# Performance work log

Measured on AMD Instinct MI355X. Metric: run time of the kernel, lower is better.

The kernel has to match this reference:

```python
import jax, jax.numpy as jnp
import numpy as np

NUM_HEADS = 16

def _alibi(S, H, dtype):
    # fairseq-style ALiBi: slopes[h] * -(|i-j|), H assumed power of 2
    start = 2.0 ** (-8.0 / H)
    slopes = start ** jnp.arange(1, H + 1, dtype=jnp.float32)      # [H]
    pos = jnp.arange(S)
    rel = -jnp.abs(pos[None, :] - pos[:, None]).astype(jnp.float32)  # [S,S]
    return (slopes[:, None, None] * rel).astype(dtype)             # [H,S,S]

def setup_inputs() -> dict:
    key = jax.random.key(0)
    kx, km, kw1, kw2 = jax.random.split(key, 4)
    B, S, D = 2, 2048, 1024
    inputs = jax.random.normal(kx, (B, S, D), dtype=jnp.float32)
    mask = jax.random.bernoulli(km, 0.9, (B, S))
    mask = mask.at[:, 0].set(True)  # ensure each row has a valid key
    Wqkv = jax.random.normal(kw1, (3 * D, D), dtype=jnp.float32) * 0.02
    bqkv = jnp.zeros((3 * D,), dtype=jnp.float32)
    Wproj = jax.random.normal(kw2, (D, D), dtype=jnp.float32) * 0.02
    bproj = jnp.zeros((D,), dtype=jnp.float32)
    return {"inputs": inputs, "mask": mask, "Wqkv": Wqkv, "bqkv": bqkv,
            "Wproj": Wproj, "bproj": bproj}

def reference(inputs, mask, Wqkv, bqkv, Wproj, bproj):
    B, S, D = inputs.shape
    H = NUM_HEADS
    dh = D // H
    scale = D ** (-0.5)  # NOTE: original scales by full dim, not head dim
    qkv = inputs @ Wqkv.T + bqkv                       # [B,S,3D]
    qkv = qkv.reshape(B, S, H, 3 * dh).transpose(0, 2, 1, 3)  # [B,H,S,3dh]
    q, k, v = qkv[..., :dh], qkv[..., dh:2 * dh], qkv[..., 2 * dh:]
    attn = jnp.einsum('bhqd,bhkd->bhqk', q, k) * scale  # [B,H,S,S]
    attn = attn + _alibi(S, H, attn.dtype)[None]
    attn = jnp.where(mask[:, None, None, :], attn, jnp.finfo(attn.dtype).min)
    attn = jax.nn.softmax(attn, axis=-1)
    x = jnp.einsum('bhqk,bhkd->bhqd', attn, v)          # [B,H,S,dh]
    x = x.transpose(0, 2, 1, 3).reshape(B, S, D)
    return x @ Wproj.T + bproj
```

## Files before the change

### kernel.cpp

```cpp
#include <hip/hip_runtime.h>
#include <cstdint>
#include <cstddef>

#define B_  2
#define S_  2048
#define D_  1024
#define H_  16
#define DH_ 64
#define M_  (B_*S_)
#define N3_ (3*D_)
#define NT_ (S_/64)

typedef float f32x4 __attribute__((ext_vector_type(4)));
typedef short short8 __attribute__((ext_vector_type(8)));
typedef unsigned short u16x8 __attribute__((ext_vector_type(8)));
typedef unsigned short u16x4 __attribute__((ext_vector_type(4)));
typedef unsigned short u16x2 __attribute__((ext_vector_type(2)));

__device__ __forceinline__ unsigned short f2bf(float x) {
    unsigned int u = __float_as_uint(x);
    unsigned int r = (u + 0x7FFFu + ((u >> 16) & 1u)) >> 16;
    return (unsigned short)r;
}

__device__ __forceinline__ float exp2_(float x) { return __builtin_amdgcn_exp2f(x); }

__device__ __forceinline__ unsigned int cvt_pk_bf16(float a, float b) {
    unsigned int r;
    asm volatile("v_cvt_pk_bf16_f32 %0, %1, %2" : "=v"(r) : "v"(a), "v"(b));
    return r;
}

__device__ __forceinline__ void gload16(const void* g, void* l) {
    __builtin_amdgcn_global_load_lds(
        (const __attribute__((address_space(1))) unsigned int*)g,
        (__attribute__((address_space(3))) unsigned int*)l,
        16, 0, 0);
}

__global__ void k_detect_mask(const unsigned char* __restrict__ mb, int* __restrict__ flag) {
    __shared__ int sBig, sM4, sM8;
    if (threadIdx.x == 0) { sBig = 0; sM4 = 0; sM8 = 0; }
    __syncthreads();
    int big = 0, m4 = 0, m8 = 0;
    for (int i = threadIdx.x; i < 4096; i += blockDim.x) {
        unsigned char v = mb[i];
        if (v > 1) big = 1;
        if (v && (i & 3)) m4 = 1;
        if (v && ((i & 7) == 4)) m8 = 1;
    }
    if (big) atomicOr(&sBig, 1);
    if (m4)  atomicOr(&sM4, 1);
    if (m8)  atomicOr(&sM8, 1);
    __syncthreads();
    if (threadIdx.x == 0) {
        int w;
        if (sBig)      w = 0;
        else if (sM4)  w = 1;
        else if (sM8)  w = 4;
        else           w = 8;
        *flag = w;
    }
}

__global__ void k_expand_mask(const void* __restrict__ mask, const int* __restrict__ flag,
                              float* __restrict__ maskbias, int n) {
    int i = blockIdx.x * blockDim.x + threadIdx.x;
    if (i >= n) return;
    int w = *flag;
    bool on;
    if (w == 0)      on = ((const float*)mask)[i] != 0.0f;
    else if (w == 1) on = ((const unsigned char*)mask)[i] != 0;
    else if (w == 4) on = ((const int*)mask)[i] != 0;
    else             on = ((const long long*)mask)[i] != 0;
    maskbias[i] = on ? 0.0f : -1e30f;
}

__global__ void k_f2bf(const float* __restrict__ in, unsigned short* __restrict__ out, int n) {
    int i = (blockIdx.x * blockDim.x + threadIdx.x) * 4;
    if (i >= n) return;
    float4 v = *reinterpret_cast<const float4*>(&in[i]);
    u16x4 o = { f2bf(v.x), f2bf(v.y), f2bf(v.z), f2bf(v.w) };
    *reinterpret_cast<u16x4*>(&out[i]) = o;
}

template <bool OUT_BF16>
__global__ __launch_bounds__(256) void k_gemm_bf16_nt(
    const unsigned short* __restrict__ A, const unsigned short* __restrict__ W,
    const float* __restrict__ bias, void* __restrict__ Cout,
    int M, int N, int K) {
    __shared__ __align__(16) unsigned short Al[128 * 64];
    __shared__ __align__(16) unsigned short Wl[128 * 64];

    const int tid  = threadIdx.x;
    const int lane = tid & 63;
    const int w    = tid >> 6;
    const int wr   = w >> 1, wc = w & 1;
    const int l16  = lane & 15, g = lane >> 4;
    const int m0 = blockIdx.y * 128, n0 = blockIdx.x * 128;

    f32x4 acc[4][4];
#pragma unroll
    for (int m = 0; m < 4; ++m)
#pragma unroll
        for (int n = 0; n < 4; ++n) acc[m][n] = (f32x4){0.f, 0.f, 0.f, 0.f};

    const int srow = tid >> 3, scol = (tid & 7) * 8;

    for (int k0 = 0; k0 < K; k0 += 64) {
        __syncthreads();
#pragma unroll
        for (int i = 0; i < 4; ++i) {
            const int c = i * 256 + tid;
            const int row = srow + i * 32;
            gload16(A + (size_t)(m0 + row) * K + k0 + scol, Al + c * 8);
            gload16(W + (size_t)(n0 + row) * K + k0 + scol, Wl + c * 8);
        }
        __syncthreads();

#pragma unroll
        for (int kk = 0; kk < 2; ++kk) {
            short8 a[4], b[4];
#pragma unroll
            for (int m = 0; m < 4; ++m)
                a[m] = *reinterpret_cast<const short8*>(
                    &Al[(size_t)(wr * 64 + m * 16 + l16) * 64 + kk * 32 + g * 8]);
#pragma unroll
            for (int n = 0; n < 4; ++n)
                b[n] = *reinterpret_cast<const short8*>(
                    &Wl[(size_t)(wc * 64 + n * 16 + l16) * 64 + kk * 32 + g * 8]);
#pragma unroll
            for (int m = 0; m < 4; ++m)
#pragma unroll
                for (int n = 0; n < 4; ++n)
                    acc[m][n] = __builtin_amdgcn_mfma_f32_16x16x32_bf16(a[m], b[n], acc[m][n], 0, 0, 0);
        }
    }

    float bv[4];
#pragma unroll
    for (int n = 0; n < 4; ++n) bv[n] = bias[n0 + wc * 64 + n * 16 + l16];
#pragma unroll
    for (int m = 0; m < 4; ++m) {
#pragma unroll
        for (int r = 0; r < 4; ++r) {
            const size_t row = m0 + wr * 64 + m * 16 + g * 4 + r;
#pragma unroll
            for (int n = 0; n < 4; ++n) {
                const int col = n0 + wc * 64 + n * 16 + l16;
                float v = acc[m][n][r] + bv[n];
                if (OUT_BF16)
                    ((unsigned short*)Cout)[row * N + col] = f2bf(v);
                else
                    ((float*)Cout)[row * N + col] = v;
            }
        }
    }
}

__global__ __launch_bounds__(512) void k_attn_mfma(
    const unsigned short* __restrict__ qkv,
    const float* __restrict__ maskbias,
    unsigned short* __restrict__ x) {
    __shared__ __align__(16) unsigned short Kt[2][64][72];
    __shared__ __align__(16) unsigned short Vt[2][64][72];
    __shared__ __align__(16) unsigned short QP[128][72];

    const int tid  = threadIdx.x;
    const int lane = tid & 63;
    const int wq   = tid >> 6;
    const int g    = lane >> 4;
    const int g4   = g * 4;
    const int l16  = lane & 15;

    const int nqt = S_ / 128;
    const int qt = blockIdx.x % nqt;
    const int h  = (blockIdx.x / nqt) % H_;
    const int b  = blockIdx.x / (nqt * H_);
    const int q0 = qt * 128;
    const size_t rowbase = (size_t)b * S_ * N3_;
    const int hq = h * 192, hk = hq + 64, hv = hq + 128;
    const unsigned short* kvb = qkv + rowbase;
    const float* mbp = maskbias + b * S_;

    {
        const int row = tid >> 2, cb = (tid & 3) * 16;
        const unsigned short* src = kvb + (size_t)(q0 + row) * N3_ + hq + cb;
        *reinterpret_cast<u16x8*>(&QP[row][cb])     = *reinterpret_cast<const u16x8*>(src);
        *reinterpret_cast<u16x8*>(&QP[row][cb + 8]) = *reinterpret_cast<const u16x8*>(src + 8);
    }

    const int krow = tid >> 3, kcb = (tid & 7) * 8;
    const int vkb = (tid & 31) * 2, vdb = (tid >> 5) * 4;
    u16x8 kr;
    u16x4 vr0, vr1;

    {
        kr  = *reinterpret_cast<const u16x8*>(kvb + (size_t)krow * N3_ + hk + kcb);
        const unsigned short* vs = kvb + (size_t)vkb * N3_ + hv + vdb;
        vr0 = *reinterpret_cast<const u16x4*>(vs);
        vr1 = *reinterpret_cast<const u16x4*>(vs + N3_);
        *reinterpret_cast<u16x8*>(&Kt[0][krow][kcb]) = kr;
#pragma unroll
        for (int j = 0; j < 4; ++j)
            *reinterpret_cast<u16x2*>(&Vt[0][vdb + j][vkb]) = (u16x2){vr0[j], vr1[j]};
    }
    __syncthreads();

    const short8 qa0 = *reinterpret_cast<const short8*>(&QP[wq*16 + l16][g*8]);
    const short8 qa1 = *reinterpret_cast<const short8*>(&QP[wq*16 + l16][32 + g*8]);

    f32x4 Oacc[4];
#pragma unroll
    for (int df = 0; df < 4; ++df) Oacc[df] = (f32x4){0.f, 0.f, 0.f, 0.f};
    float m = -1e30f, l = 0.0f;

    const float LOG2E = 1.4426950408889634f;
    const float c1 = 0.03125f * LOG2E;
    const float c2 = exp2f(-0.5f * (float)(h + 1)) * LOG2E;
    const int   qw0 = q0 + wq * 16;
    const int   qg  = qw0 + l16;
    float albr[4];
#pragma unroll
    for (int r = 0; r < 4; ++r) albr[r] = c2 * (float)(g4 + r);
    const float c2_16 = c2 * 16.0f;

    for (int t = 0; t < NT_; ++t) {
        const int k0 = t * 64;
        const int cur = t & 1;

        if (t + 1 < NT_) {
            const int kn = k0 + 64;
            kr  = *reinterpret_cast<const u16x8*>(kvb + (size_t)(kn + krow) * N3_ + hk + kcb);
            const unsigned short* vs = kvb + (size_t)(kn + vkb) * N3_ + hv + vdb;
            vr0 = *reinterpret_cast<const u16x4*>(vs);
            vr1 = *reinterpret_cast<const u16x4*>(vs + N3_);
        }

        f32x4 amv[4];
#pragma unroll
        for (int jb = 0; jb < 4; ++jb)
            amv[jb] = *reinterpret_cast<const f32x4*>(&mbp[k0 + jb * 16 + g4]);

        float p_[4][4];
        __builtin_amdgcn_s_setprio(1);
#pragma unroll
        for (int jb = 0; jb < 4; ++jb) {
            short8 kb0 = *reinterpret_cast<const short8*>(&Kt[cur][jb*16 + l16][g*8]);
            short8 kb1 = *reinterpret_cast<const short8*>(&Kt[cur][jb*16 + l16][32 + g*8]);
            f32x4 c = (f32x4){0.f, 0.f, 0.f, 0.f};
            c = __builtin_amdgcn_mfma_f32_16x16x32_bf16(kb0, qa0, c, 0, 0, 0);
            c = __builtin_amdgcn_mfma_f32_16x16x32_bf16(kb1, qa1, c, 0, 0, 0);
#pragma unroll
            for (int r = 0; r < 4; ++r) p_[jb][r] = c[r];
        }
        __builtin_amdgcn_s_setprio(0);

        if (k0 + 64 <= qw0) {
            const float tb = c2 * (float)(k0 - qg);
#pragma unroll
            for (int jb = 0; jb < 4; ++jb) {
                const float tbj = tb + c2_16 * (float)jb;
#pragma unroll
                for (int r = 0; r < 4; ++r)
                    p_[jb][r] = fmaf(p_[jb][r], c1, tbj + albr[r] + amv[jb][r]);
            }
        } else if (k0 >= qw0 + 16) {
            const float tb = c2 * (float)(k0 - qg);
#pragma unroll
            for (int jb = 0; jb < 4; ++jb) {
                const float tbj = -tb - c2_16 * (float)jb;
#pragma unroll
                for (int r = 0; r < 4; ++r)
                    p_[jb][r] = fmaf(p_[jb][r], c1, tbj - albr[r] + amv[jb][r]);
            }
        } else {
            const int dbase = k0 - qg;
#pragma unroll
            for (int jb = 0; jb < 4; ++jb)
#pragma unroll
                for (int r = 0; r < 4; ++r) {
                    int d = dbase + jb * 16 + g4 + r;
                    d = d < 0 ? -d : d;
                    p_[jb][r] = fmaf(p_[jb][r], c1, amv[jb][r] - c2 * (float)d);
                }
        }

        float mx;
        {
            float m0_ = fmaxf(fmaxf(p_[0][0], p_[0][1]), fmaxf(p_[0][2], p_[0][3]));
            float m1_ = fmaxf(fmaxf(p_[1][0], p_[1][1]), fmaxf(p_[1][2], p_[1][3]));
            float m2_ = fmaxf(fmaxf(p_[2][0], p_[2][1]), fmaxf(p_[2][2], p_[2][3]));
            float m3_ = fmaxf(fmaxf(p_[3][0], p_[3][1]), fmaxf(p_[3][2], p_[3][3]));
            mx = fmaxf(fmaxf(m0_, m1_), fmaxf(m2_, m3_));
        }
        mx = fmaxf(mx, __shfl_xor(mx, 16));
        mx = fmaxf(mx, __shfl_xor(mx, 32));

        if (__any(mx > m + 8.0f)) {
            const float mn = fmaxf(m, mx);
            const float cr = exp2_(m - mn);
            m = mn;
            l *= cr;
            const int srcb = (lane & 48) + ((lane & 48) >> 2);
#pragma unroll
            for (int r = 0; r < 4; ++r) {
                const float crq = __shfl(cr, srcb + r);
#pragma unroll
                for (int df = 0; df < 4; ++df) Oacc[df][r] *= crq;
            }
        }

        float ps = 0.0f;
#pragma unroll
        for (int jb = 0; jb < 4; ++jb)
#pragma unroll
            for (int r = 0; r < 4; ++r) {
                float p = exp2_(p_[jb][r] - m);
                p_[jb][r] = p;
                ps += p;
            }

#pragma unroll
        for (int jb = 0; jb < 4; ++jb) {
            uint2 st;
            st.x = cvt_pk_bf16(p_[jb][0], p_[jb][1]);
            st.y = cvt_pk_bf16(p_[jb][2], p_[jb][3]);
            *reinterpret_cast<uint2*>(&QP[wq*16 + l16][jb*16 + g4]) = st;
        }

        const short8 pa0 = *reinterpret_cast<const short8*>(&QP[wq*16 + l16][g*8]);
        const short8 pa1 = *reinterpret_cast<const short8*>(&QP[wq*16 + l16][32 + g*8]);
        __builtin_amdgcn_s_setprio(1);
#pragma unroll
        for (int df = 0; df < 4; ++df) {
            short8 vb0 = *reinterpret_cast<const short8*>(&Vt[cur][df*16 + l16][g*8]);
            short8 vb1 = *reinterpret_cast<const short8*>(&Vt[cur][df*16 + l16][32 + g*8]);
            Oacc[df] = __builtin_amdgcn_mfma_f32_16x16x32_bf16(pa0, vb0, Oacc[df], 0, 0, 0);
            Oacc[df] = __builtin_amdgcn_mfma_f32_16x16x32_bf16(pa1, vb1, Oacc[df], 0, 0, 0);
        }
        __builtin_amdgcn_s_setprio(0);

        ps += __shfl_xor(ps, 16);
        ps += __shfl_xor(ps, 32);
        l += ps;

        if (t + 1 < NT_) {
            *reinterpret_cast<u16x8*>(&Kt[cur ^ 1][krow][kcb]) = kr;
#pragma unroll
            for (int j = 0; j < 4; ++j)
                *reinterpret_cast<u16x2*>(&Vt[cur ^ 1][vdb + j][vkb]) = (u16x2){vr0[j], vr1[j]};
            __syncthreads();
        }
    }

    const int srcb = (lane & 48) + ((lane & 48) >> 2);
    float invq[4];
#pragma unroll
    for (int r = 0; r < 4; ++r) invq[r] = 1.0f / __shfl(l, srcb + r);
#pragma unroll
    for (int df = 0; df < 4; ++df) {
#pragma unroll
        for (int r = 0; r < 4; ++r) {
            const int qrow = q0 + wq * 16 + g4 + r;
            x[(size_t)(b * S_ + qrow) * D_ + h * 64 + df * 16 + l16] = f2bf(Oacc[df][r] * invq[r]);
        }
    }
}

extern "C" void kernel_launch(void* const* d_in, const int* in_sizes, int n_in,
                              void* d_out, int out_size, void* d_ws, size_t ws_size,
                              hipStream_t stream) {
    const float* inputs = (const float*)d_in[0];
    const void*  mask   = d_in[1];
    const float* Wqkv   = (const float*)d_in[2];
    const float* bqkv   = (const float*)d_in[3];
    const float* Wproj  = (const float*)d_in[4];
    const float* bproj  = (const float*)d_in[5];
    float* out = (float*)d_out;

    unsigned short* qkvb = (unsigned short*)d_ws;
    unsigned short* xb   = qkvb + (size_t)M_ * N3_;
    unsigned short* Ab   = xb + (size_t)M_ * D_;
    unsigned short* Wqb  = Ab + (size_t)M_ * D_;
    unsigned short* Wpb  = Wqb + (size_t)N3_ * D_;
    float* maskbias = (float*)(Wpb + (size_t)D_ * D_);
    int*   flag     = (int*)(maskbias + M_);

    k_detect_mask<<<1, 256, 0, stream>>>((const unsigned char*)mask, flag);
    k_expand_mask<<<(M_ + 255) / 256, 256, 0, stream>>>(mask, flag, maskbias, M_);

    k_f2bf<<<(M_ * D_ / 4 + 255) / 256, 256, 0, stream>>>(inputs, Ab, M_ * D_);
    k_f2bf<<<(N3_ * D_ / 4 + 255) / 256, 256, 0, stream>>>(Wqkv, Wqb, N3_ * D_);
    k_f2bf<<<(D_ * D_ / 4 + 255) / 256, 256, 0, stream>>>(Wproj, Wpb, D_ * D_);

    dim3 g1(N3_ / 128, M_ / 128);
    k_gemm_bf16_nt<true><<<g1, 256, 0, stream>>>(Ab, Wqb, bqkv, qkvb, M_, N3_, D_);

    k_attn_mfma<<<B_ * H_ * (S_ / 128), 512, 0, stream>>>(qkvb, maskbias, xb);

    dim3 g2(D_ / 128, M_ / 128);
    k_gemm_bf16_nt<false><<<g2, 256, 0, stream>>>(xb, Wpb, bproj, out, M_, D_, D_);
}
```

Before: 178.2 us.

## Software-pipeline QK^T one tile ahead in attention, add XCD swizzle and occupancy hint

Restructures the attention loop so the QK^T MFMAs for tile t+1 are issued while softmax and PV for tile t run. This adds a third V buffer and moves the K/V register prefetch to just after the barrier. Workgroup IDs in both the GEMM and attention kernels are remapped with an XCD-aware swizzle so neighbouring tiles share an L2. The attention kernel also gets a launch_bounds min-blocks hint of 4. The aim is to hide MFMA latency behind the softmax math and improve cache locality, at the cost of more registers and LDS.

```diff
diff --git a/kernel.cpp b/kernel.cpp
--- a/kernel.cpp
+++ b/kernel.cpp
@@ -29,6 +29,11 @@
     unsigned int r;
     asm volatile("v_cvt_pk_bf16_f32 %0, %1, %2" : "=v"(r) : "v"(a), "v"(b));
     return r;
+}
+
+__device__ __forceinline__ int xcd_swizzle(int lin, int nwg) {
+    const int cpx = nwg >> 3;
+    return (lin & 7) * cpx + (lin >> 3);
 }
 
 __device__ __forceinline__ void gload16(const void* g, void* l) {
@@ -97,7 +102,11 @@
     const int w    = tid >> 6;
     const int wr   = w >> 1, wc = w & 1;
     const int l16  = lane & 15, g = lane >> 4;
-    const int m0 = blockIdx.y * 128, n0 = blockIdx.x * 128;
+
+    const int nwg = gridDim.x * gridDim.y;
+    int lin = blockIdx.y * gridDim.x + blockIdx.x;
+    lin = xcd_swizzle(lin, nwg);
+    const int m0 = (lin / gridDim.x) * 128, n0 = (lin % gridDim.x) * 128;
 
     f32x4 acc[4][4];
 #pragma unroll
@@ -158,12 +167,12 @@
     }
 }
 
-__global__ __launch_bounds__(512) void k_attn_mfma(
+__global__ __launch_bounds__(512, 4) void k_attn_mfma(
     const unsigned short* __restrict__ qkv,
     const float* __restrict__ maskbias,
     unsigned short* __restrict__ x) {
     __shared__ __align__(16) unsigned short Kt[2][64][72];
-    __shared__ __align__(16) unsigned short Vt[2][64][72];
+    __shared__ __align__(16) unsigned short Vt[3][64][72];
     __shared__ __align__(16) unsigned short QP[128][72];
 
     const int tid  = threadIdx.x;
@@ -174,9 +183,11 @@
     const int l16  = lane & 15;
 
     const int nqt = S_ / 128;
-    const int qt = blockIdx.x % nqt;
-    const int h  = (blockIdx.x / nqt) % H_;
-    const int b  = blockIdx.x / (nqt * H_);
+    const int nwg = B_ * H_ * nqt;
+    const int bid = xcd_swizzle(blockIdx.x, nwg);
+    const int qt = bid % nqt;
+    const int h  = (bid / nqt) % H_;
+    const int b  = bid / (nqt * H_);
     const int q0 = qt * 128;
     const size_t rowbase = (size_t)b * S_ * N3_;
     const int hq = h * 192, hk = hq + 64, hv = hq + 128;
@@ -225,29 +236,19 @@
     for (int r = 0; r < 4; ++r) albr[r] = c2 * (float)(g4 + r);
     const float c2_16 = c2 * 16.0f;
 
-    for (int t = 0; t < NT_; ++t) {
-        const int k0 = t * 64;
-        const int cur = t & 1;
-
-        if (t + 1 < NT_) {
-            const int kn = k0 + 64;
-            kr  = *reinterpret_cast<const u16x8*>(kvb + (size_t)(kn + krow) * N3_ + hk + kcb);
-            const unsigned short* vs = kvb + (size_t)(kn + vkb) * N3_ + hv + vdb;
-            vr0 = *reinterpret_cast<const u16x4*>(vs);
-            vr1 = *reinterpret_cast<const u16x4*>(vs + N3_);
-        }
-
-        f32x4 amv[4];
-#pragma unroll
-        for (int jb = 0; jb < 4; ++jb)
-            amv[jb] = *reinterpret_cast<const f32x4*>(&mbp[k0 + jb * 16 + g4]);
-
-        float p_[4][4];
+    float p_[4][4];
+
+    {
+        kr  = *reinterpret_cast<const u16x8*>(kvb + (size_t)(64 + krow) * N3_ + hk + kcb);
+        const unsigned short* vs = kvb + (size_t)(64 + vkb) * N3_ + hv + vdb;
+        vr0 = *reinterpret_cast<const u16x4*>(vs);
+        vr1 = *reinterpret_cast<const u16x4*>(vs + N3_);
+
         __builtin_amdgcn_s_setprio(1);
 #pragma unroll
         for (int jb = 0; jb < 4; ++jb) {
-            short8 kb0 = *reinterpret_cast<const short8*>(&Kt[cur][jb*16 + l16][g*8]);
-            short8 kb1 = *reinterpret_cast<const short8*>(&Kt[cur][jb*16 + l16][32 + g*8]);
+            short8 kb0 = *reinterpret_cast<const short8*>(&Kt[0][jb*16 + l16][g*8]);
+            short8 kb1 = *reinterpret_cast<const short8*>(&Kt[0][jb*16 + l16][32 + g*8]);
             f32x4 c = (f32x4){0.f, 0.f, 0.f, 0.f};
             c = __builtin_amdgcn_mfma_f32_16x16x32_bf16(kb0, qa0, c, 0, 0, 0);
             c = __builtin_amdgcn_mfma_f32_16x16x32_bf16(kb1, qa1, c, 0, 0, 0);
@@ -256,8 +257,48 @@
         }
         __builtin_amdgcn_s_setprio(0);
 
-        if (k0 + 64 <= qw0) {
-            const float tb = c2 * (float)(k0 - qg);
+        *reinterpret_cast<u16x8*>(&Kt[1][krow][kcb]) = kr;
+#pragma unroll
+        for (int j = 0; j < 4; ++j)
+            *reinterpret_cast<u16x2*>(&Vt[1][vdb + j][vkb]) = (u16x2){vr0[j], vr1[j]};
+    }
+    __syncthreads();
+    {
+        kr  = *reinterpret_cast<const u16x8*>(kvb + (size_t)(128 + krow) * N3_ + hk + kcb);
+        const unsigned short* vs = kvb + (size_t)(128 + vkb) * N3_ + hv + vdb;
+        vr0 = *reinterpret_cast<const u16x4*>(vs);
+        vr1 = *reinterpret_cast<const u16x4*>(vs + N3_);
+    }
+
+    int vb_r = 0;
+    int vb_w = 2;
+
+    for (int t = 1; t < NT_ + 1; ++t) {
+        const int k0m = (t - 1) * 64;
+
+        f32x4 amv[4];
+#pragma unroll
+        for (int jb = 0; jb < 4; ++jb)
+            amv[jb] = *reinterpret_cast<const f32x4*>(&mbp[k0m + jb * 16 + g4]);
+
+        f32x4 cnx[4];
+        if (t < NT_) {
+            const unsigned short (*Kc)[72] = Kt[t & 1];
+            __builtin_amdgcn_s_setprio(1);
+#pragma unroll
+            for (int jb = 0; jb < 4; ++jb) {
+                short8 kb0 = *reinterpret_cast<const short8*>(&Kc[jb*16 + l16][g*8]);
+                short8 kb1 = *reinterpret_cast<const short8*>(&Kc[jb*16 + l16][32 + g*8]);
+                f32x4 c = (f32x4){0.f, 0.f, 0.f, 0.f};
+                c = __builtin_amdgcn_mfma_f32_16x16x32_bf16(kb0, qa0, c, 0, 0, 0);
+                c = __builtin_amdgcn_mfma_f32_16x16x32_bf16(kb1, qa1, c, 0, 0, 0);
+                cnx[jb] = c;
+            }
+            __builtin_amdgcn_s_setprio(0);
+        }
+
+        if (k0m + 64 <= qw0) {
+            const float tb = c2 * (float)(k0m - qg);
 #pragma unroll
             for (int jb = 0; jb < 4; ++jb) {
                 const float tbj = tb + c2_16 * (float)jb;
@@ -265,8 +306,8 @@
                 for (int r = 0; r < 4; ++r)
                     p_[jb][r] = fmaf(p_[jb][r], c1, tbj + albr[r] + amv[jb][r]);
             }
-        } else if (k0 >= qw0 + 16) {
-            const float tb = c2 * (float)(k0 - qg);
+        } else if (k0m >= qw0 + 16) {
+            const float tb = c2 * (float)(k0m - qg);
 #pragma unroll
             for (int jb = 0; jb < 4; ++jb) {
                 const float tbj = -tb - c2_16 * (float)jb;
@@ -275,7 +316,7 @@
                     p_[jb][r] = fmaf(p_[jb][r], c1, tbj - albr[r] + amv[jb][r]);
             }
         } else {
-            const int dbase = k0 - qg;
+            const int dbase = k0m - qg;
 #pragma unroll
             for (int jb = 0; jb < 4; ++jb)
 #pragma unroll
@@ -329,28 +370,47 @@
             *reinterpret_cast<uint2*>(&QP[wq*16 + l16][jb*16 + g4]) = st;
         }
 
-        const short8 pa0 = *reinterpret_cast<const short8*>(&QP[wq*16 + l16][g*8]);
-        const short8 pa1 = *reinterpret_cast<const short8*>(&QP[wq*16 + l16][32 + g*8]);
-        __builtin_amdgcn_s_setprio(1);
-#pragma unroll
-        for (int df = 0; df < 4; ++df) {
-            short8 vb0 = *reinterpret_cast<const short8*>(&Vt[cur][df*16 + l16][g*8]);
-            short8 vb1 = *reinterpret_cast<const short8*>(&Vt[cur][df*16 + l16][32 + g*8]);
-            Oacc[df] = __builtin_amdgcn_mfma_f32_16x16x32_bf16(pa0, vb0, Oacc[df], 0, 0, 0);
-            Oacc[df] = __builtin_amdgcn_mfma_f32_16x16x32_bf16(pa1, vb1, Oacc[df], 0, 0, 0);
-        }
-        __builtin_amdgcn_s_setprio(0);
+        {
+            const short8 pa0 = *reinterpret_cast<const short8*>(&QP[wq*16 + l16][g*8]);
+            const short8 pa1 = *reinterpret_cast<const short8*>(&QP[wq*16 + l16][32 + g*8]);
+            const unsigned short (*Vc)[72] = Vt[vb_r];
+            __builtin_amdgcn_s_setprio(1);
+#pragma unroll
+            for (int df = 0; df < 4; ++df) {
+                short8 vb0 = *reinterpret_cast<const short8*>(&Vc[df*16 + l16][g*8]);
+                short8 vb1 = *reinterpret_cast<const short8*>(&Vc[df*16 + l16][32 + g*8]);
+                Oacc[df] = __builtin_amdgcn_mfma_f32_16x16x32_bf16(pa0, vb0, Oacc[df], 0, 0, 0);
+                Oacc[df] = __builtin_amdgcn_mfma_f32_16x16x32_bf16(pa1, vb1, Oacc[df], 0, 0, 0);
+            }
+            __builtin_amdgcn_s_setprio(0);
+        }
 
         ps += __shfl_xor(ps, 16);
         ps += __shfl_xor(ps, 32);
         l += ps;
 
         if (t + 1 < NT_) {
-            *reinterpret_cast<u16x8*>(&Kt[cur ^ 1][krow][kcb]) = kr;
+            *reinterpret_cast<u16x8*>(&Kt[(t + 1) & 1][krow][kcb]) = kr;
 #pragma unroll
             for (int j = 0; j < 4; ++j)
-                *reinterpret_cast<u16x2*>(&Vt[cur ^ 1][vdb + j][vkb]) = (u16x2){vr0[j], vr1[j]};
+                *reinterpret_cast<u16x2*>(&Vt[vb_w][vdb + j][vkb]) = (u16x2){vr0[j], vr1[j]};
             __syncthreads();
+            if (t + 2 < NT_) {
+                const int kn = (t + 2) * 64;
+                kr  = *reinterpret_cast<const u16x8*>(kvb + (size_t)(kn + krow) * N3_ + hk + kcb);
+                const unsigned short* vs = kvb + (size_t)(kn + vkb) * N3_ + hv + vdb;
+                vr0 = *reinterpret_cast<const u16x4*>(vs);
+                vr1 = *reinterpret_cast<const u16x4*>(vs + N3_);
+            }
+        }
+        vb_r = (vb_r == 2) ? 0 : vb_r + 1;
+        vb_w = (vb_w == 2) ? 0 : vb_w + 1;
+
+        if (t < NT_) {
+#pragma unroll
+            for (int jb = 0; jb < 4; ++jb)
+#pragma unroll
+                for (int r = 0; r < 4; ++r) p_[jb][r] = cnx[jb][r];
         }
     }
 
```

After: 178.5 us. About the same (+0.2%).
